# Kernel optimization log

Hardware: AMD Instinct MI355X
Metric: run time of the kernel (lower is better)

Reference implementation:

```python
import jax, jax.numpy as jnp
import numpy as np

N_NODES = 20000
N_EDGES = 400000
IN_DIM = 512
OUT_DIM = 1
HIDDEN = [512, 512, 512, 256, OUT_DIM]


def _glorot(key, fan_in, fan_out):
    lim = np.sqrt(6.0 / (fan_in + fan_out)).astype(np.float32)
    return jax.random.uniform(key, (fan_in, fan_out), jnp.float32, -lim, lim)


def setup_inputs() -> dict:
    key = jax.random.key(0)
    ks = jax.random.split(key, 16)
    x = jax.random.normal(ks[0], (N_NODES, IN_DIM), jnp.float32)
    edge_index = jax.random.randint(ks[1], (2, N_EDGES), 0, N_NODES, jnp.int64)
    edge_attr = jax.random.uniform(ks[2], (N_EDGES,), jnp.float32)
    inp = {"x": x, "edge_index": edge_index, "edge_attr": edge_attr}
    dims = [IN_DIM] + HIDDEN
    for i in range(5):
        inp[f"W{i+1}"] = _glorot(ks[3 + i], dims[i], dims[i + 1])
        inp[f"b{i+1}"] = jnp.zeros((dims[i + 1],), jnp.float32)
    return inp


def gcn_layer(x, W, b, src, dst, ew, n):
    # x: [N, Fin] -> [N, Fout]; GCNConv: D^{-1/2}(A+I)D^{-1/2} X W + b
    h = x @ W
    loop = jnp.arange(n)
    src_f = jnp.concatenate([src, loop])
    dst_f = jnp.concatenate([dst, loop])
    ew_f = jnp.concatenate([ew, jnp.ones((n,), x.dtype)])  # self-loop weight 1
    deg = jax.ops.segment_sum(ew_f, dst_f, num_segments=n)
    dinv = jnp.where(deg > 0, jax.lax.rsqrt(deg), 0.0)
    norm = dinv[src_f] * ew_f * dinv[dst_f]  # [E+N]
    out = jax.ops.segment_sum(norm[:, None] * h[src_f], dst_f, num_segments=n)
    return out + b


def reference(x, edge_index, edge_attr, W1, b1, W2, b2, W3, b3, W4, b4, W5, b5):
    src, dst = edge_index[0], edge_index[1]
    n = x.shape[0]
    h = jax.nn.relu(gcn_layer(x, W1, b1, src, dst, edge_attr, n))
    h = jax.nn.relu(gcn_layer(h, W2, b2, src, dst, edge_attr, n))
    h = jax.nn.relu(gcn_layer(h, W3, b3, src, dst, edge_attr, n))
    h = jax.nn.relu(gcn_layer(h, W4, b4, src, dst, edge_attr, n))
    h = gcn_layer(h, W5, b5, src, dst, edge_attr, n)
    return h
```

## Files before the change

kernel.cpp:

```cpp
#include <hip/hip_runtime.h>
#include <cstdint>
#include <cstddef>

#define N_NODES 20000
#define N_EDGES 400000
#define NBLK 79

typedef __attribute__((ext_vector_type(8))) short bf16x8;
typedef __attribute__((ext_vector_type(4))) float f32x4;

__device__ __forceinline__ float bf2f(unsigned short u) {
    return __uint_as_float(((unsigned int)u) << 16);
}
__device__ __forceinline__ unsigned short f2bf(float f) {
    unsigned int x = __float_as_uint(f);
    unsigned int lsb = (x >> 16) & 1u;
    x += 0x7fffu + lsb;
    return (unsigned short)(x >> 16);
}

__device__ __forceinline__ float ldF(const void* p, size_t i, bool bf) {
    return bf ? bf2f(((const unsigned short*)p)[i]) : ((const float*)p)[i];
}

__device__ __forceinline__ void gl2lds16(const unsigned short* g, unsigned short* l) {
    __builtin_amdgcn_global_load_lds(
        (const __attribute__((address_space(1))) void*)g,
        (__attribute__((address_space(3))) void*)l, 16, 0, 0);
}

__global__ void k_detect(const unsigned int* __restrict__ xw, const int* __restrict__ raw,
                         int* __restrict__ flag) {
    int lane = threadIdx.x;
    int cnt = 0, nz = 0;
    for (int i = lane; i < 256; i += 64) {
        unsigned short lo = (unsigned short)(xw[i] & 0xffffu);
        int e = (lo >> 7) & 0xff;
        if (e >= 110 && e <= 135) cnt++;
    }
    for (int i = 2 * lane + 1; i < 512; i += 128)
        if (raw[i] != 0) nz++;
#pragma unroll
    for (int off = 32; off > 0; off >>= 1) {
        cnt += __shfl_down(cnt, off);
        nz  += __shfl_down(nz, off);
    }
    if (lane == 0) {
        flag[0] = (cnt >= 128) ? 1 : 0;
        flag[1] = (nz == 0) ? 1 : 0;
    }
}

__global__ void k_canon_deg(const int* __restrict__ raw, const void* __restrict__ ew,
                            const int* __restrict__ flagp,
                            int* __restrict__ src32, int* __restrict__ dst32,
                            float* __restrict__ deg, int* __restrict__ counts) {
    bool bf = (flagp[0] != 0);
    int is64 = flagp[1];
    int e = blockIdx.x * blockDim.x + threadIdx.x;
    if (e >= N_EDGES) return;
    int s, d;
    if (is64) { s = raw[2 * e]; d = raw[2 * (N_EDGES + e)]; }
    else      { s = raw[e];     d = raw[N_EDGES + e]; }
    src32[e] = s;
    dst32[e] = d;
    atomicAdd(&deg[d], ldF(ew, e, bf));
    atomicAdd(&counts[d], 1);
}

__global__ __launch_bounds__(256) void k_part(const int* __restrict__ counts,
                                              const float* __restrict__ deg,
                                              float* __restrict__ dinv,
                                              float* __restrict__ selfnorm,
                                              int* __restrict__ bsum) {
    __shared__ int s[256];
    int t = threadIdx.x;
    int i = blockIdx.x * 256 + t;
    int c = (i < N_NODES) ? counts[i] : 0;
    if (i < N_NODES) {
        float d = deg[i] + 1.0f;
        float r = rsqrtf(d);
        dinv[i] = r;
        selfnorm[i] = r * r;
    }
    s[t] = c;
    __syncthreads();
    for (int off = 128; off > 0; off >>= 1) {
        if (t < off) s[t] += s[t + off];
        __syncthreads();
    }
    if (t == 0) bsum[blockIdx.x] = s[0];
}

__global__ void k_scanb(const int* __restrict__ bsum, int* __restrict__ bofs,
                        int* __restrict__ rowptr) {
    __shared__ int s[128];
    int t = threadIdx.x;
    int v = (t < NBLK) ? bsum[t] : 0;
    s[t] = v;
    __syncthreads();
    for (int off = 1; off < 128; off <<= 1) {
        int u = (t >= off) ? s[t - off] : 0;
        __syncthreads();
        s[t] += u;
        __syncthreads();
    }
    if (t < NBLK) bofs[t] = s[t] - v;
    if (t == NBLK - 1) rowptr[N_NODES] = s[t];
}

__global__ __launch_bounds__(256) void k_row(const int* __restrict__ counts,
                                             const int* __restrict__ bofs,
                                             int* __restrict__ rowptr) {
    __shared__ int s[256];
    int t = threadIdx.x;
    int b = blockIdx.x;
    int i = b * 256 + t;
    int c = (i < N_NODES) ? counts[i] : 0;
    s[t] = c;
    __syncthreads();
    for (int off = 1; off < 256; off <<= 1) {
        int u = (t >= off) ? s[t - off] : 0;
        __syncthreads();
        s[t] += u;
        __syncthreads();
    }
    if (i < N_NODES) rowptr[i] = bofs[b] + s[t] - c;
}

__global__ void k_csr(const int* __restrict__ src, const int* __restrict__ dst,
                      const void* __restrict__ ew, const int* __restrict__ flagp,
                      const float* __restrict__ dinv, const int* __restrict__ rowptr,
                      int* __restrict__ fill, int* __restrict__ csr_src,
                      float* __restrict__ csr_norm) {
    bool bf = (*flagp != 0);
    int e = blockIdx.x * blockDim.x + threadIdx.x;
    if (e >= N_EDGES) return;
    int s = src[e], d = dst[e];
    int p = rowptr[d] + atomicAdd(&fill[d], 1);
    csr_src[p] = s;
    csr_norm[p] = dinv[s] * ldF(ew, e, bf) * dinv[d];
}

__global__ void k_cast_in(const void* __restrict__ x, const int* __restrict__ flagp,
                          unsigned short* __restrict__ out, int n4) {
    bool bf = (*flagp != 0);
    int i = blockIdx.x * blockDim.x + threadIdx.x;
    if (i >= n4) return;
    if (bf) {
        ((uint2*)out)[i] = ((const uint2*)x)[i];
    } else {
        float4 v = ((const float4*)x)[i];
        unsigned int lo = (unsigned int)f2bf(v.x) | ((unsigned int)f2bf(v.y) << 16);
        unsigned int hi = (unsigned int)f2bf(v.z) | ((unsigned int)f2bf(v.w) << 16);
        ((uint2*)out)[i] = make_uint2(lo, hi);
    }
}

__global__ void k_pack_all(const void* __restrict__ W1, const void* __restrict__ W2,
                           const void* __restrict__ W3, const void* __restrict__ W4,
                           const int* __restrict__ flagp, unsigned short* __restrict__ Wp) {
    bool bf = (*flagp != 0);
    int gidx = blockIdx.x * 256 + threadIdx.x;
    if (gidx >= 114688) return;
    const void* W;
    int idx = gidx, N, nbl;
    if (gidx < 32768)      { W = W1; N = 512; nbl = 5; }
    else if (gidx < 65536) { W = W2; N = 512; nbl = 5; idx -= 32768; }
    else if (gidx < 98304) { W = W3; N = 512; nbl = 5; idx -= 65536; }
    else                   { W = W4; N = 256; nbl = 4; idx -= 98304; }
    int lane = idx & 63;
    int blk = idx >> 6;
    int nb = blk & ((1 << nbl) - 1);
    int kb = blk >> nbl;
    int n = (nb << 4) + (lane & 15);
    int kbase = (kb << 5) + ((lane >> 4) << 3);
    unsigned short o[8];
#pragma unroll
    for (int j = 0; j < 8; ++j)
        o[j] = f2bf(ldF(W, (size_t)(kbase + j) * N + n, bf));
    *(uint4*)(&Wp[(size_t)gidx * 8]) = *(const uint4*)o;
}

__global__ void k_castb(const void* __restrict__ b1, const void* __restrict__ b2,
                        const void* __restrict__ b3, const void* __restrict__ b4,
                        const int* __restrict__ flagp, float* __restrict__ biasf) {
    bool bf = (*flagp != 0);
    int i = blockIdx.x * blockDim.x + threadIdx.x;
    if (i >= 2048) return;
    int L = i >> 9, r = i & 511;
    if (L == 3 && r >= 256) return;
    const void* b = (L == 0) ? b1 : (L == 1) ? b2 : (L == 2) ? b3 : b4;
    biasf[i] = ldF(b, r, bf);
}

__global__ __launch_bounds__(256) void k_gemm_mfma(const unsigned short* __restrict__ A,
                                                   const unsigned short* __restrict__ Bp,
                                                   unsigned short* __restrict__ C,
                                                   int M, int K, int N) {
    const int AP = 40;
    __shared__ __align__(16) unsigned short As[128 * AP];
    __shared__ __align__(16) unsigned short Bs[8 * 512];
    int tid = threadIdx.x;
    int lane = tid & 63;
    int wave = tid >> 6;
    int wr = wave >> 1, wc = wave & 1;
    int row0 = blockIdx.x * 128;
    int col0 = blockIdx.y * 128;
    int nbt = N >> 4;
    int q = lane >> 4;
    int mm = lane & 15;

    f32x4 acc[4][4] = {};

    for (int kb = 0; kb < (K >> 5); ++kb) {
        const unsigned short* breg = Bp + (((size_t)kb * nbt + (col0 >> 4)) << 9);
        gl2lds16(breg + (size_t)tid * 8, &Bs[(size_t)tid * 8]);
        gl2lds16(breg + (size_t)(tid + 256) * 8, &Bs[(size_t)(tid + 256) * 8]);
#pragma unroll
        for (int i = 0; i < 2; ++i) {
            int c = tid + i * 256;
            int row = c >> 2, kq = c & 3;
            int grow = row0 + row;
            uint4 v = make_uint4(0u, 0u, 0u, 0u);
            if (grow < M)
                v = *(const uint4*)(&A[(size_t)grow * K + (kb << 5) + (kq << 3)]);
            *(uint4*)(&As[row * AP + (kq << 3)]) = v;
        }
        __syncthreads();
        bf16x8 af[4], bfr[4];
#pragma unroll
        for (int mb = 0; mb < 4; ++mb)
            af[mb] = *(const bf16x8*)(&As[(wr * 64 + mb * 16 + mm) * AP + q * 8]);
#pragma unroll
        for (int nb = 0; nb < 4; ++nb)
            bfr[nb] = *(const bf16x8*)(&Bs[((wc * 4 + nb) * 64 + lane) * 8]);
#pragma unroll
        for (int mb = 0; mb < 4; ++mb)
#pragma unroll
            for (int nb = 0; nb < 4; ++nb)
                acc[mb][nb] = __builtin_amdgcn_mfma_f32_16x16x32_bf16(
                    af[mb], bfr[nb], acc[mb][nb], 0, 0, 0);
        __syncthreads();
    }
#pragma unroll
    for (int mb = 0; mb < 4; ++mb) {
#pragma unroll
        for (int r = 0; r < 4; ++r) {
            int grow = row0 + wr * 64 + mb * 16 + q * 4 + r;
            if (grow < M) {
#pragma unroll
                for (int nb = 0; nb < 4; ++nb) {
                    int gcol = col0 + wc * 64 + nb * 16 + mm;
                    C[(size_t)grow * N + gcol] = f2bf(acc[mb][nb][r]);
                }
            }
        }
    }
}

template <int W>
__device__ __forceinline__ void ldrow(const unsigned short* h, size_t row, int F, int lane,
                                      unsigned int* u) {
    const unsigned int* p = (const unsigned int*)(h + row * F) + lane * W;
    if constexpr (W == 4) {
        uint4 v = *(const uint4*)p; u[0] = v.x; u[1] = v.y; u[2] = v.z; u[3] = v.w;
    } else {
        uint2 v = *(const uint2*)p; u[0] = v.x; u[1] = v.y;
    }
}
template <int W>
__device__ __forceinline__ void fmarow(const unsigned int* u, float w, float* acc) {
#pragma unroll
    for (int k = 0; k < W; ++k) {
        acc[2 * k]     = fmaf(bf2f((unsigned short)(u[k] & 0xffffu)), w, acc[2 * k]);
        acc[2 * k + 1] = fmaf(bf2f((unsigned short)(u[k] >> 16)),     w, acc[2 * k + 1]);
    }
}

template <int F, int FPL>
__global__ __launch_bounds__(256) void k_agg_w(const unsigned short* __restrict__ h,
                                               const int* __restrict__ rowptr,
                                               const int* __restrict__ csr_src,
                                               const float* __restrict__ csr_norm,
                                               const float* __restrict__ selfnorm,
                                               const float* __restrict__ biasf,
                                               unsigned short* __restrict__ out,
                                               int relu) {
    constexpr int W = FPL / 2;
    int lane = threadIdx.x & 63;
    int wave = threadIdx.x >> 6;
    int node = blockIdx.x * 4 + wave;
    if (node >= N_NODES) return;
    int e0 = rowptr[node], e1 = rowptr[node + 1];
    float sn = selfnorm[node];

    float acc[FPL];
    {
        unsigned int u[W];
        ldrow<W>(h, (size_t)node, F, lane, u);
#pragma unroll
        for (int k = 0; k < W; ++k) {
            acc[2 * k]     = sn * bf2f((unsigned short)(u[k] & 0xffffu));
            acc[2 * k + 1] = sn * bf2f((unsigned short)(u[k] >> 16));
        }
    }
    int j = e0;
    for (; j + 3 < e1; j += 4) {
        int s0 = csr_src[j], s1 = csr_src[j + 1], s2 = csr_src[j + 2], s3 = csr_src[j + 3];
        float w0 = csr_norm[j], w1 = csr_norm[j + 1], w2 = csr_norm[j + 2], w3 = csr_norm[j + 3];
        unsigned int u0[W], u1[W], u2[W], u3[W];
        ldrow<W>(h, (size_t)s0, F, lane, u0);
        ldrow<W>(h, (size_t)s1, F, lane, u1);
        ldrow<W>(h, (size_t)s2, F, lane, u2);
        ldrow<W>(h, (size_t)s3, F, lane, u3);
        fmarow<W>(u0, w0, acc);
        fmarow<W>(u1, w1, acc);
        fmarow<W>(u2, w2, acc);
        fmarow<W>(u3, w3, acc);
    }
    for (; j < e1; ++j) {
        int s0 = csr_src[j];
        float w0 = csr_norm[j];
        unsigned int u0[W];
        ldrow<W>(h, (size_t)s0, F, lane, u0);
        fmarow<W>(u0, w0, acc);
    }
    {
        const float* bp = biasf + lane * FPL;
#pragma unroll
        for (int k = 0; k < FPL; ++k) acc[k] += bp[k];
        if (relu) {
#pragma unroll
            for (int k = 0; k < FPL; ++k) acc[k] = fmaxf(acc[k], 0.f);
        }
        unsigned int o[W];
#pragma unroll
        for (int k = 0; k < W; ++k)
            o[k] = (unsigned int)f2bf(acc[2 * k]) | ((unsigned int)f2bf(acc[2 * k + 1]) << 16);
        unsigned int* q = (unsigned int*)(out + (size_t)node * F) + lane * W;
        if constexpr (W == 4) { *(uint4*)q = make_uint4(o[0], o[1], o[2], o[3]); }
        else                  { *(uint2*)q = make_uint2(o[0], o[1]); }
    }
}

__global__ __launch_bounds__(256) void k_gemv(const unsigned short* __restrict__ A,
                                              const void* __restrict__ W,
                                              const int* __restrict__ flagp,
                                              float* __restrict__ out, int K) {
    bool bf = (*flagp != 0);
    int wave = threadIdx.x >> 6, lane = threadIdx.x & 63;
    int row = blockIdx.x * 4 + wave;
    if (row >= N_NODES) return;
    float s = 0.f;
    for (int k = lane; k < K; k += 64) s += bf2f(A[(size_t)row * K + k]) * ldF(W, k, bf);
#pragma unroll
    for (int off = 32; off > 0; off >>= 1) s += __shfl_down(s, off);
    if (lane == 0) out[row] = s;
}

__global__ void k_final(const float* __restrict__ h5, const int* __restrict__ rowptr,
                        const int* __restrict__ csr_src, const float* __restrict__ csr_norm,
                        const float* __restrict__ selfnorm,
                        const void* __restrict__ b5, const int* __restrict__ flagp,
                        void* __restrict__ out) {
    bool bf = (*flagp != 0);
    int i = blockIdx.x * blockDim.x + threadIdx.x;
    if (i >= N_NODES) return;
    float acc = selfnorm[i] * h5[i];
    int e0 = rowptr[i], e1 = rowptr[i + 1];
    for (int j = e0; j < e1; ++j) acc += csr_norm[j] * h5[csr_src[j]];
    acc += ldF(b5, 0, bf);
    if (bf) ((unsigned short*)out)[i] = f2bf(acc);
    else    ((float*)out)[i] = acc;
}

extern "C" void kernel_launch(void* const* d_in, const int* in_sizes, int n_in,
                              void* d_out, int out_size, void* d_ws, size_t ws_size,
                              hipStream_t stream) {
    const void* x  = d_in[0];
    const int*  ei = (const int*)d_in[1];
    const void* ea = d_in[2];
    const void* W1 = d_in[3];
    const void* b1 = d_in[4];
    const void* W2 = d_in[5];
    const void* b2 = d_in[6];
    const void* W3 = d_in[7];
    const void* b3 = d_in[8];
    const void* W4 = d_in[9];
    const void* b4 = d_in[10];
    const void* W5 = d_in[11];
    const void* b5 = d_in[12];

    char* ws = (char*)d_ws;
    size_t off = 0;
    auto take = [&](size_t bytes) -> void* {
        off = (off + 255) & ~(size_t)255;
        void* p = ws + off;
        off += bytes;
        return p;
    };
    int*   flagp    = (int*)take(2 * sizeof(int));
    float* deg      = (float*)take(N_NODES * sizeof(float));
    int*   counts   = (int*)take(N_NODES * sizeof(int));
    int*   fill     = (int*)take(N_NODES * sizeof(int));
    size_t zspan    = (size_t)((char*)(fill + N_NODES) - (char*)deg);
    float* dinv     = (float*)take(N_NODES * sizeof(float));
    float* selfnorm = (float*)take(N_NODES * sizeof(float));
    float* h5       = (float*)take(N_NODES * sizeof(float));
    float* biasf    = (float*)take(4 * 512 * sizeof(float));
    int*   bsum     = (int*)take(128 * sizeof(int));
    int*   bofs     = (int*)take(128 * sizeof(int));
    int*   rowptr   = (int*)take((N_NODES + 1) * sizeof(int));
    int*   src32    = (int*)take(N_EDGES * sizeof(int));
    int*   dst32    = (int*)take(N_EDGES * sizeof(int));
    int*   csr_src  = (int*)take(N_EDGES * sizeof(int));
    float* csr_norm = (float*)take(N_EDGES * sizeof(float));
    unsigned short* Wp = (unsigned short*)take((size_t)114688 * 8 * sizeof(unsigned short));
    unsigned short* P  = (unsigned short*)take((size_t)N_NODES * 512 * sizeof(unsigned short));
    unsigned short* H  = (unsigned short*)take((size_t)N_NODES * 512 * sizeof(unsigned short));

    hipMemsetAsync(deg, 0, zspan, stream);

    const int EB = (N_EDGES + 255) / 256;
    const int NB = (N_NODES + 255) / 256;
    const int AGB = (N_NODES + 3) / 4;

    k_detect<<<1, 64, 0, stream>>>((const unsigned int*)x, ei, flagp);
    k_canon_deg<<<EB, 256, 0, stream>>>(ei, ea, flagp, src32, dst32, deg, counts);
    k_part<<<NB, 256, 0, stream>>>(counts, deg, dinv, selfnorm, bsum);
    k_scanb<<<1, 128, 0, stream>>>(bsum, bofs, rowptr);
    k_row<<<NB, 256, 0, stream>>>(counts, bofs, rowptr);
    k_csr<<<EB, 256, 0, stream>>>(src32, dst32, ea, flagp, dinv, rowptr, fill, csr_src, csr_norm);

    const int n4 = (N_NODES * 512) / 4;
    k_cast_in<<<(n4 + 255) / 256, 256, 0, stream>>>(x, flagp, P, n4);
    k_pack_all<<<(114688 + 255) / 256, 256, 0, stream>>>(W1, W2, W3, W4, flagp, Wp);
    k_castb<<<8, 256, 0, stream>>>(b1, b2, b3, b4, flagp, biasf);

    const int MB128 = (N_NODES + 127) / 128;

    k_gemm_mfma<<<dim3(MB128, 4), 256, 0, stream>>>(P, Wp, H, N_NODES, 512, 512);
    k_agg_w<512, 8><<<AGB, 256, 0, stream>>>(H, rowptr, csr_src, csr_norm, selfnorm,
                                             biasf, P, 1);
    k_gemm_mfma<<<dim3(MB128, 4), 256, 0, stream>>>(P, Wp + (size_t)32768 * 8, H,
                                                    N_NODES, 512, 512);
    k_agg_w<512, 8><<<AGB, 256, 0, stream>>>(H, rowptr, csr_src, csr_norm, selfnorm,
                                             biasf + 512, P, 1);
    k_gemm_mfma<<<dim3(MB128, 4), 256, 0, stream>>>(P, Wp + (size_t)65536 * 8, H,
                                                    N_NODES, 512, 512);
    k_agg_w<512, 8><<<AGB, 256, 0, stream>>>(H, rowptr, csr_src, csr_norm, selfnorm,
                                             biasf + 1024, P, 1);
    k_gemm_mfma<<<dim3(MB128, 2), 256, 0, stream>>>(P, Wp + (size_t)98304 * 8, H,
                                                    N_NODES, 512, 256);
    k_agg_w<256, 4><<<AGB, 256, 0, stream>>>(H, rowptr, csr_src, csr_norm, selfnorm,
                                             biasf + 1536, P, 1);

    k_gemv<<<(N_NODES + 3) / 4, 256, 0, stream>>>(P, W5, flagp, h5, 256);
    k_final<<<NB, 256, 0, stream>>>(h5, rowptr, csr_src, csr_norm, selfnorm, b5, flagp,
                                    d_out);
}
```

Before: 484.3 us.

## Merge prep kernels, drop LDS staging in GEMM, fuse last aggregation with GEMV

```diff
diff --git a/kernel.cpp b/kernel.cpp
--- a/kernel.cpp
+++ b/kernel.cpp
@@ -5,6 +5,7 @@
 #define N_NODES 20000
 #define N_EDGES 400000
 #define NBLK 79
+#define MPAD 20128
 
 typedef __attribute__((ext_vector_type(8))) short bf16x8;
 typedef __attribute__((ext_vector_type(4))) float f32x4;
@@ -21,12 +22,6 @@
 
 __device__ __forceinline__ float ldF(const void* p, size_t i, bool bf) {
     return bf ? bf2f(((const unsigned short*)p)[i]) : ((const float*)p)[i];
-}
-
-__device__ __forceinline__ void gl2lds16(const unsigned short* g, unsigned short* l) {
-    __builtin_amdgcn_global_load_lds(
-        (const __attribute__((address_space(1))) void*)g,
-        (__attribute__((address_space(3))) void*)l, 16, 0, 0);
 }
 
 __global__ void k_detect(const unsigned int* __restrict__ xw, const int* __restrict__ raw,
@@ -142,65 +137,71 @@
     csr_norm[p] = dinv[s] * ldF(ew, e, bf) * dinv[d];
 }
 
-__global__ void k_cast_in(const void* __restrict__ x, const int* __restrict__ flagp,
-                          unsigned short* __restrict__ out, int n4) {
+__global__ __launch_bounds__(256) void k_prep(const void* __restrict__ x,
+                                              const void* __restrict__ W1,
+                                              const void* __restrict__ W2,
+                                              const void* __restrict__ W3,
+                                              const void* __restrict__ W4,
+                                              const void* __restrict__ b1,
+                                              const void* __restrict__ b2,
+                                              const void* __restrict__ b3,
+                                              const void* __restrict__ b4,
+                                              const void* __restrict__ W5,
+                                              const int* __restrict__ flagp,
+                                              unsigned short* __restrict__ P,
+                                              unsigned short* __restrict__ Wp,
+                                              float* __restrict__ biasf) {
     bool bf = (*flagp != 0);
-    int i = blockIdx.x * blockDim.x + threadIdx.x;
-    if (i >= n4) return;
-    if (bf) {
-        ((uint2*)out)[i] = ((const uint2*)x)[i];
+    int b = blockIdx.x;
+    int t = threadIdx.x;
+    if (b < 10000) {
+        int i = b * 256 + t;
+        if (bf) {
+            ((uint2*)P)[i] = ((const uint2*)x)[i];
+        } else {
+            float4 v = ((const float4*)x)[i];
+            unsigned int lo = (unsigned int)f2bf(v.x) | ((unsigned int)f2bf(v.y) << 16);
+            unsigned int hi = (unsigned int)f2bf(v.z) | ((unsigned int)f2bf(v.w) << 16);
+            ((uint2*)P)[i] = make_uint2(lo, hi);
+        }
+    } else if (b < 10448) {
+        int gidx = (b - 10000) * 256 + t;
+        if (gidx >= 114688) return;
+        const void* W;
+        int idx = gidx, N, nbl;
+        if (gidx < 32768)      { W = W1; N = 512; nbl = 5; }
+        else if (gidx < 65536) { W = W2; N = 512; nbl = 5; idx -= 32768; }
+        else if (gidx < 98304) { W = W3; N = 512; nbl = 5; idx -= 65536; }
+        else                   { W = W4; N = 256; nbl = 4; idx -= 98304; }
+        int lane = idx & 63;
+        int blk = idx >> 6;
+        int nb = blk & ((1 << nbl) - 1);
+        int kb = blk >> nbl;
+        int n = (nb << 4) + (lane & 15);
+        int kbase = (kb << 5) + ((lane >> 4) << 3);
+        unsigned short o[8];
+#pragma unroll
+        for (int j = 0; j < 8; ++j)
+            o[j] = f2bf(ldF(W, (size_t)(kbase + j) * N + n, bf));
+        *(uint4*)(&Wp[(size_t)gidx * 8]) = *(const uint4*)o;
     } else {
-        float4 v = ((const float4*)x)[i];
-        unsigned int lo = (unsigned int)f2bf(v.x) | ((unsigned int)f2bf(v.y) << 16);
-        unsigned int hi = (unsigned int)f2bf(v.z) | ((unsigned int)f2bf(v.w) << 16);
-        ((uint2*)out)[i] = make_uint2(lo, hi);
-    }
-}
-
-__global__ void k_pack_all(const void* __restrict__ W1, const void* __restrict__ W2,
-                           const void* __restrict__ W3, const void* __restrict__ W4,
-                           const int* __restrict__ flagp, unsigned short* __restrict__ Wp) {
-    bool bf = (*flagp != 0);
-    int gidx = blockIdx.x * 256 + threadIdx.x;
-    if (gidx >= 114688) return;
-    const void* W;
-    int idx = gidx, N, nbl;
-    if (gidx < 32768)      { W = W1; N = 512; nbl = 5; }
-    else if (gidx < 65536) { W = W2; N = 512; nbl = 5; idx -= 32768; }
-    else if (gidx < 98304) { W = W3; N = 512; nbl = 5; idx -= 65536; }
-    else                   { W = W4; N = 256; nbl = 4; idx -= 98304; }
-    int lane = idx & 63;
-    int blk = idx >> 6;
-    int nb = blk & ((1 << nbl) - 1);
-    int kb = blk >> nbl;
-    int n = (nb << 4) + (lane & 15);
-    int kbase = (kb << 5) + ((lane >> 4) << 3);
-    unsigned short o[8];
-#pragma unroll
-    for (int j = 0; j < 8; ++j)
-        o[j] = f2bf(ldF(W, (size_t)(kbase + j) * N + n, bf));
-    *(uint4*)(&Wp[(size_t)gidx * 8]) = *(const uint4*)o;
-}
-
-__global__ void k_castb(const void* __restrict__ b1, const void* __restrict__ b2,
-                        const void* __restrict__ b3, const void* __restrict__ b4,
-                        const int* __restrict__ flagp, float* __restrict__ biasf) {
-    bool bf = (*flagp != 0);
-    int i = blockIdx.x * blockDim.x + threadIdx.x;
-    if (i >= 2048) return;
-    int L = i >> 9, r = i & 511;
-    if (L == 3 && r >= 256) return;
-    const void* b = (L == 0) ? b1 : (L == 1) ? b2 : (L == 2) ? b3 : b4;
-    biasf[i] = ldF(b, r, bf);
+        int i = (b - 10448) * 256 + t;
+        if (i >= 2304) return;
+        if (i < 2048) {
+            int L = i >> 9, r = i & 511;
+            if (L == 3 && r >= 256) return;
+            const void* bb = (L == 0) ? b1 : (L == 1) ? b2 : (L == 2) ? b3 : b4;
+            biasf[i] = ldF(bb, r, bf);
+        } else {
+            biasf[i] = ldF(W5, i - 2048, bf);
+        }
+    }
 }
 
 __global__ __launch_bounds__(256) void k_gemm_mfma(const unsigned short* __restrict__ A,
                                                    const unsigned short* __restrict__ Bp,
                                                    unsigned short* __restrict__ C,
                                                    int M, int K, int N) {
-    const int AP = 40;
-    __shared__ __align__(16) unsigned short As[128 * AP];
-    __shared__ __align__(16) unsigned short Bs[8 * 512];
     int tid = threadIdx.x;
     int lane = tid & 63;
     int wave = tid >> 6;
@@ -210,38 +211,30 @@
     int nbt = N >> 4;
     int q = lane >> 4;
     int mm = lane & 15;
+    int cb0 = (col0 >> 4) + wc * 4;
+
+    const unsigned short* aptr[4];
+#pragma unroll
+    for (int mb = 0; mb < 4; ++mb)
+        aptr[mb] = A + (size_t)(row0 + wr * 64 + mb * 16 + mm) * K + q * 8;
+    const unsigned short* bptr = Bp + ((size_t)cb0 * 64 + lane) * 8;
 
     f32x4 acc[4][4] = {};
 
     for (int kb = 0; kb < (K >> 5); ++kb) {
-        const unsigned short* breg = Bp + (((size_t)kb * nbt + (col0 >> 4)) << 9);
-        gl2lds16(breg + (size_t)tid * 8, &Bs[(size_t)tid * 8]);
-        gl2lds16(breg + (size_t)(tid + 256) * 8, &Bs[(size_t)(tid + 256) * 8]);
-#pragma unroll
-        for (int i = 0; i < 2; ++i) {
-            int c = tid + i * 256;
-            int row = c >> 2, kq = c & 3;
-            int grow = row0 + row;
-            uint4 v = make_uint4(0u, 0u, 0u, 0u);
-            if (grow < M)
-                v = *(const uint4*)(&A[(size_t)grow * K + (kb << 5) + (kq << 3)]);
-            *(uint4*)(&As[row * AP + (kq << 3)]) = v;
-        }
-        __syncthreads();
         bf16x8 af[4], bfr[4];
 #pragma unroll
         for (int mb = 0; mb < 4; ++mb)
-            af[mb] = *(const bf16x8*)(&As[(wr * 64 + mb * 16 + mm) * AP + q * 8]);
+            af[mb] = *(const bf16x8*)(aptr[mb] + kb * 32);
 #pragma unroll
         for (int nb = 0; nb < 4; ++nb)
-            bfr[nb] = *(const bf16x8*)(&Bs[((wc * 4 + nb) * 64 + lane) * 8]);
+            bfr[nb] = *(const bf16x8*)(bptr + ((size_t)kb * nbt + nb) * 512);
 #pragma unroll
         for (int mb = 0; mb < 4; ++mb)
 #pragma unroll
             for (int nb = 0; nb < 4; ++nb)
                 acc[mb][nb] = __builtin_amdgcn_mfma_f32_16x16x32_bf16(
                     af[mb], bfr[nb], acc[mb][nb], 0, 0, 0);
-        __syncthreads();
     }
 #pragma unroll
     for (int mb = 0; mb < 4; ++mb) {
@@ -278,16 +271,14 @@
     }
 }
 
-template <int F, int FPL>
 __global__ __launch_bounds__(256) void k_agg_w(const unsigned short* __restrict__ h,
                                                const int* __restrict__ rowptr,
                                                const int* __restrict__ csr_src,
                                                const float* __restrict__ csr_norm,
                                                const float* __restrict__ selfnorm,
                                                const float* __restrict__ biasf,
-                                               unsigned short* __restrict__ out,
-                                               int relu) {
-    constexpr int W = FPL / 2;
+                                               unsigned short* __restrict__ out) {
+    constexpr int F = 512, FPL = 8, W = 4;
     int lane = threadIdx.x & 63;
     int wave = threadIdx.x >> 6;
     int node = blockIdx.x * 4 + wave;
@@ -329,34 +320,73 @@
     {
         const float* bp = biasf + lane * FPL;
 #pragma unroll
-        for (int k = 0; k < FPL; ++k) acc[k] += bp[k];
-        if (relu) {
-#pragma unroll
-            for (int k = 0; k < FPL; ++k) acc[k] = fmaxf(acc[k], 0.f);
-        }
+        for (int k = 0; k < FPL; ++k) acc[k] = fmaxf(acc[k] + bp[k], 0.f);
         unsigned int o[W];
 #pragma unroll
         for (int k = 0; k < W; ++k)
             o[k] = (unsigned int)f2bf(acc[2 * k]) | ((unsigned int)f2bf(acc[2 * k + 1]) << 16);
-        unsigned int* q = (unsigned int*)(out + (size_t)node * F) + lane * W;
-        if constexpr (W == 4) { *(uint4*)q = make_uint4(o[0], o[1], o[2], o[3]); }
-        else                  { *(uint2*)q = make_uint2(o[0], o[1]); }
-    }
-}
-
-__global__ __launch_bounds__(256) void k_gemv(const unsigned short* __restrict__ A,
-                                              const void* __restrict__ W,
-                                              const int* __restrict__ flagp,
-                                              float* __restrict__ out, int K) {
-    bool bf = (*flagp != 0);
-    int wave = threadIdx.x >> 6, lane = threadIdx.x & 63;
-    int row = blockIdx.x * 4 + wave;
-    if (row >= N_NODES) return;
-    float s = 0.f;
-    for (int k = lane; k < K; k += 64) s += bf2f(A[(size_t)row * K + k]) * ldF(W, k, bf);
-#pragma unroll
-    for (int off = 32; off > 0; off >>= 1) s += __shfl_down(s, off);
-    if (lane == 0) out[row] = s;
+        *(uint4*)((unsigned int*)(out + (size_t)node * F) + lane * W) =
+            make_uint4(o[0], o[1], o[2], o[3]);
+    }
+}
+
+__global__ __launch_bounds__(256) void k_agg_fuse(const unsigned short* __restrict__ h,
+                                                  const int* __restrict__ rowptr,
+                                                  const int* __restrict__ csr_src,
+                                                  const float* __restrict__ csr_norm,
+                                                  const float* __restrict__ selfnorm,
+                                                  const float* __restrict__ biasf,
+                                                  const float* __restrict__ w5f,
+                                                  float* __restrict__ h5) {
+    constexpr int F = 256, FPL = 4, W = 2;
+    int lane = threadIdx.x & 63;
+    int wave = threadIdx.x >> 6;
+    int node = blockIdx.x * 4 + wave;
+    if (node >= N_NODES) return;
+    int e0 = rowptr[node], e1 = rowptr[node + 1];
+    float sn = selfnorm[node];
+
+    float acc[FPL];
+    {
+        unsigned int u[W];
+        ldrow<W>(h, (size_t)node, F, lane, u);
+#pragma unroll
+        for (int k = 0; k < W; ++k) {
+            acc[2 * k]     = sn * bf2f((unsigned short)(u[k] & 0xffffu));
+            acc[2 * k + 1] = sn * bf2f((unsigned short)(u[k] >> 16));
+        }
+    }
+    int j = e0;
+    for (; j + 3 < e1; j += 4) {
+        int s0 = csr_src[j], s1 = csr_src[j + 1], s2 = csr_src[j + 2], s3 = csr_src[j + 3];
+        float w0 = csr_norm[j], w1 = csr_norm[j + 1], w2 = csr_norm[j + 2], w3 = csr_norm[j + 3];
+        unsigned int u0[W], u1[W], u2[W], u3[W];
+        ldrow<W>(h, (size_t)s0, F, lane, u0);
+        ldrow<W>(h, (size_t)s1, F, lane, u1);
+        ldrow<W>(h, (size_t)s2, F, lane, u2);
+        ldrow<W>(h, (size_t)s3, F, lane, u3);
+        fmarow<W>(u0, w0, acc);
+        fmarow<W>(u1, w1, acc);
+        fmarow<W>(u2, w2, acc);
+        fmarow<W>(u3, w3, acc);
+    }
+    for (; j < e1; ++j) {
+        int s0 = csr_src[j];
+        float w0 = csr_norm[j];
+        unsigned int u0[W];
+        ldrow<W>(h, (size_t)s0, F, lane, u0);
+        fmarow<W>(u0, w0, acc);
+    }
+    const float* bp = biasf + lane * FPL;
+    const float* wp = w5f + lane * FPL;
+    float partial = 0.f;
+#pragma unroll
+    for (int k = 0; k < FPL; ++k)
+        partial += fmaxf(acc[k] + bp[k], 0.f) * wp[k];
+#pragma unroll
+    for (int off = 32; off > 0; off >>= 1)
+        partial += __shfl_xor(partial, off);
+    if (lane == 0) h5[node] = partial;
 }
 
 __global__ void k_final(const float* __restrict__ h5, const int* __restrict__ rowptr,
@@ -408,7 +438,7 @@
     float* dinv     = (float*)take(N_NODES * sizeof(float));
     float* selfnorm = (float*)take(N_NODES * sizeof(float));
     float* h5       = (float*)take(N_NODES * sizeof(float));
-    float* biasf    = (float*)take(4 * 512 * sizeof(float));
+    float* biasf    = (float*)take(2304 * sizeof(float));
     int*   bsum     = (int*)take(128 * sizeof(int));
     int*   bofs     = (int*)take(128 * sizeof(int));
     int*   rowptr   = (int*)take((N_NODES + 1) * sizeof(int));
@@ -417,8 +447,8 @@
     int*   csr_src  = (int*)take(N_EDGES * sizeof(int));
     float* csr_norm = (float*)take(N_EDGES * sizeof(float));
     unsigned short* Wp = (unsigned short*)take((size_t)114688 * 8 * sizeof(unsigned short));
-    unsigned short* P  = (unsigned short*)take((size_t)N_NODES * 512 * sizeof(unsigned short));
-    unsigned short* H  = (unsigned short*)take((size_t)N_NODES * 512 * sizeof(unsigned short));
+    unsigned short* P  = (unsigned short*)take((size_t)MPAD * 512 * sizeof(unsigned short));
+    unsigned short* H  = (unsigned short*)take((size_t)MPAD * 512 * sizeof(unsigned short));
 
     hipMemsetAsync(deg, 0, zspan, stream);
 
@@ -433,30 +463,24 @@
     k_row<<<NB, 256, 0, stream>>>(counts, bofs, rowptr);
     k_csr<<<EB, 256, 0, stream>>>(src32, dst32, ea, flagp, dinv, rowptr, fill, csr_src, csr_norm);
 
-    const int n4 = (N_NODES * 512) / 4;
-    k_cast_in<<<(n4 + 255) / 256, 256, 0, stream>>>(x, flagp, P, n4);
-    k_pack_all<<<(114688 + 255) / 256, 256, 0, stream>>>(W1, W2, W3, W4, flagp, Wp);
-    k_castb<<<8, 256, 0, stream>>>(b1, b2, b3, b4, flagp, biasf);
+    k_prep<<<10457, 256, 0, stream>>>(x, W1, W2, W3, W4, b1, b2, b3, b4, W5, flagp,
+                                      P, Wp, biasf);
 
     const int MB128 = (N_NODES + 127) / 128;
 
     k_gemm_mfma<<<dim3(MB128, 4), 256, 0, stream>>>(P, Wp, H, N_NODES, 512, 512);
-    k_agg_w<512, 8><<<AGB, 256, 0, stream>>>(H, rowptr, csr_src, csr_norm, selfnorm,
-                                             biasf, P, 1);
+    k_agg_w<<<AGB, 256, 0, stream>>>(H, rowptr, csr_src, csr_norm, selfnorm, biasf, P);
     k_gemm_mfma<<<dim3(MB128, 4), 256, 0, stream>>>(P, Wp + (size_t)32768 * 8, H,
                                                     N_NODES, 512, 512);
-    k_agg_w<512, 8><<<AGB, 256, 0, stream>>>(H, rowptr, csr_src, csr_norm, selfnorm,
-                                             biasf + 512, P, 1);
+    k_agg_w<<<AGB, 256, 0, stream>>>(H, rowptr, csr_src, csr_norm, selfnorm, biasf + 512, P);
     k_gemm_mfma<<<dim3(MB128, 4), 256, 0, stream>>>(P, Wp + (size_t)65536 * 8, H,
                                                     N_NODES, 512, 512);
-    k_agg_w<512, 8><<<AGB, 256, 0, stream>>>(H, rowptr, csr_src, csr_norm, selfnorm,
-                                             biasf + 1024, P, 1);
+    k_agg_w<<<AGB, 256, 0, stream>>>(H, rowptr, csr_src, csr_norm, selfnorm, biasf + 1024, P);
     k_gemm_mfma<<<dim3(MB128, 2), 256, 0, stream>>>(P, Wp + (size_t)98304 * 8, H,
                                                     N_NODES, 512, 256);
-    k_agg_w<256, 4><<<AGB, 256, 0, stream>>>(H, rowptr, csr_src, csr_norm, selfnorm,
-                                             biasf + 1536, P, 1);
-
-    k_gemv<<<(N_NODES + 3) / 4, 256, 0, stream>>>(P, W5, flagp, h5, 256);
+    k_agg_fuse<<<AGB, 256, 0, stream>>>(H, rowptr, csr_src, csr_norm, selfnorm,
+                                        biasf + 1536, biasf + 2048, h5);
+
     k_final<<<NB, 256, 0, stream>>>(h5, rowptr, csr_src, csr_norm, selfnorm, b5, flagp,
                                     d_out);
 }
```

After: 502.0 us. 1.04x slower.
